# Kernel optimization log

Hardware: AMD Instinct MI355X
Metric: run time of the kernel (lower is better)

## Reference

```python
import jax, jax.numpy as jnp
import numpy as np

N, M, D = 131072, 128, 128

def setup_inputs() -> dict:
    key = jax.random.key(0)
    k1, k2, k3 = jax.random.split(key, 3)
    X = jax.random.normal(k1, (N, D), dtype=jnp.float32)
    r = jax.random.uniform(k2, (N, M), dtype=jnp.float32)
    mus = jax.random.normal(k3, (M, D), dtype=jnp.float32)
    return {"X": X, "r": r, "mus": mus}

def reference(X, r, mus):
    # Squared pairwise L2 distances without materializing [N, M, D]:
    x2 = jnp.sum(X * X, axis=1)            # [N]
    mu2 = jnp.sum(mus * mus, axis=1)       # [M]
    cross = X @ mus.T                      # [N, M]
    dist2 = jnp.maximum(x2[:, None] + mu2[None, :] - 2.0 * cross, 0.0)
    loss = jnp.sum(r * dist2) / X.shape[0]
    return loss
```

## Files before the change

### kernel.cpp

```cpp
#include <hip/hip_runtime.h>
#include <hip/hip_bf16.h>


typedef __attribute__((ext_vector_type(8)))  short  short8;
typedef __attribute__((ext_vector_type(16))) float  float16v;

#define LDSP 136

#if defined(__has_builtin)
#if __has_builtin(__builtin_amdgcn_cvt_pk_bf16_f32)
#define HAVE_PK_BF16 1
#endif
#endif

__device__ __forceinline__ unsigned int pk_bf16(float x, float y) {
#ifdef HAVE_PK_BF16
    typedef __attribute__((ext_vector_type(2))) __bf16 bf16x2;
    bf16x2 p = __builtin_amdgcn_cvt_pk_bf16_f32(x, y);
    return __builtin_bit_cast(unsigned int, p);
#else
    unsigned int ux = __float_as_uint(x);
    unsigned int uy = __float_as_uint(y);
    ux += 0x7fffu + ((ux >> 16) & 1u);
    uy += 0x7fffu + ((uy >> 16) & 1u);
    return (ux >> 16) | (uy & 0xffff0000u);
#endif
}

__global__ void zero_ws_kernel(float* ws) { ws[threadIdx.x] = 0.0f; }

__global__ void final_reduce_kernel(const float* ws, float* out) {
    const int lane = threadIdx.x;
    float t = ws[lane];
    #pragma unroll
    for (int off = 32; off > 0; off >>= 1) t += __shfl_down(t, off);
    if (lane == 0) out[0] = t * (1.0f / 131072.0f);
}

__global__ __launch_bounds__(256, 3)
void isoloss_kernel(const float* __restrict__ X,
                    const float* __restrict__ r,
                    const float* __restrict__ mus,
                    float* __restrict__ ws)
{
    const int tid  = threadIdx.x;
    const int blk  = blockIdx.x;
    const int wave = tid >> 6;
    const int lane = tid & 63;
    const int col  = lane & 31;
    const int half = lane >> 5;

    __shared__ unsigned short ldsA[128 * LDSP];
    __shared__ float x2s[128];
    __shared__ float wsum[4];

    const float* xbase = X + (size_t)blk * 128 * 128;
    float4 xv[16];
    #pragma unroll
    for (int it = 0; it < 16; ++it)
        xv[it] = *(const float4*)(xbase + (size_t)(it * 256 + tid) * 4);

    #pragma unroll
    for (int it = 0; it < 16; ++it) {
        const float4 v = xv[it];
        float p = v.x*v.x + v.y*v.y + v.z*v.z + v.w*v.w;
        p += __shfl_xor(p, 16);
        p += __shfl_xor(p, 8);
        p += __shfl_xor(p, 4);
        p += __shfl_xor(p, 2);
        p += __shfl_xor(p, 1);
        const int row = it * 8 + (tid >> 5);
        if ((tid & 31) == 0) x2s[row] = p;
        uint2 h;
        h.x = pk_bf16(v.x, v.y);
        h.y = pk_bf16(v.z, v.w);
        *(uint2*)&ldsA[row * LDSP + (tid & 31) * 4] = h;
    }

    short8 bfrag[8];
    float mu2p = 0.0f;
    {
        const float* mrow = mus + (size_t)(wave * 32 + col) * 128 + half * 8;
        #pragma unroll
        for (int ks = 0; ks < 8; ++ks) {
            const float4 a = *(const float4*)(mrow + ks * 16);
            const float4 b = *(const float4*)(mrow + ks * 16 + 4);
            mu2p += a.x*a.x + a.y*a.y + a.z*a.z + a.w*a.w
                  + b.x*b.x + b.y*b.y + b.z*b.z + b.w*b.w;
            union { short8 s8; uint4 u4; } u;
            u.u4.x = pk_bf16(a.x, a.y);
            u.u4.y = pk_bf16(a.z, a.w);
            u.u4.z = pk_bf16(b.x, b.y);
            u.u4.w = pk_bf16(b.z, b.w);
            bfrag[ks] = u.s8;
        }
    }
    const float mu2 = mu2p + __shfl_xor(mu2p, 32);

    __syncthreads();

    float s = 0.0f;
    #pragma unroll
    for (int mt = 0; mt < 4; ++mt) {
        const float* rp = r + (size_t)(blk * 128 + mt * 32) * 128 + wave * 32 + col;
        float rv[16];
        #pragma unroll
        for (int reg = 0; reg < 16; ++reg) {
            const int rl = (reg & 3) + 8 * (reg >> 2) + 4 * half;
            rv[reg] = rp[(size_t)rl * 128];
        }

        float16v acc = {};
        #pragma unroll
        for (int ks = 0; ks < 8; ++ks) {
            const short8 af = *(const short8*)&ldsA[(mt * 32 + col) * LDSP + ks * 16 + half * 8];
            acc = __builtin_amdgcn_mfma_f32_32x32x16_bf16(af, bfrag[ks], acc, 0, 0, 0);
        }

        float4 xq[4];
        #pragma unroll
        for (int q = 0; q < 4; ++q)
            xq[q] = *(const float4*)&x2s[mt * 32 + q * 8 + half * 4];

        #pragma unroll
        for (int reg = 0; reg < 16; ++reg) {
            const float d = fmaxf(xq[reg >> 2][reg & 3] + mu2 - 2.0f * acc[reg], 0.0f);
            s += rv[reg] * d;
        }
    }

    #pragma unroll
    for (int off = 32; off > 0; off >>= 1) s += __shfl_down(s, off);
    if (lane == 0) wsum[wave] = s;
    __syncthreads();
    if (tid == 0)
        atomicAdd(&ws[blk & 63], wsum[0] + wsum[1] + wsum[2] + wsum[3]);
}

extern "C" void kernel_launch(void* const* d_in, const int* in_sizes, int n_in,
                              void* d_out, int out_size, void* d_ws, size_t ws_size,
                              hipStream_t stream) {
    const float* X   = (const float*)d_in[0];
    const float* r   = (const float*)d_in[1];
    const float* mus = (const float*)d_in[2];
    float* out = (float*)d_out;
    float* ws  = (float*)d_ws;

    zero_ws_kernel<<<1, 64, 0, stream>>>(ws);
    isoloss_kernel<<<1024, 256, 0, stream>>>(X, r, mus, ws);
    final_reduce_kernel<<<1, 64, 0, stream>>>(ws, out);
}
```

Before: 151.0 us.

## Software-pipeline X/r loads across 32-row groups with double-buffered LDS

Replaces the up-front load of the whole 128x128 X tile with a loop over four 32-row groups. Each group uses a double-buffered LDS slice, and the next group's X and r are prefetched while the current group runs its MFMAs. The MFMA operands are swapped so that r can be read as contiguous float4 vectors, and a barrier that waits only on LDS (not on outstanding global loads) lets those loads stay in flight. LDS use drops and launch bounds rise to 4 blocks per CU for more occupancy, at the cost of more barriers per block and tighter register limits.

```diff
diff --git a/kernel.cpp b/kernel.cpp
--- a/kernel.cpp
+++ b/kernel.cpp
@@ -27,6 +27,13 @@
 #endif
 }
 
+__device__ __forceinline__ void barrier_lgkm_only() {
+    asm volatile("" ::: "memory");
+    __builtin_amdgcn_s_waitcnt(0xC07F);
+    __builtin_amdgcn_s_barrier();
+    asm volatile("" ::: "memory");
+}
+
 __global__ void zero_ws_kernel(float* ws) { ws[threadIdx.x] = 0.0f; }
 
 __global__ void final_reduce_kernel(const float* ws, float* out) {
@@ -37,7 +44,7 @@
     if (lane == 0) out[0] = t * (1.0f / 131072.0f);
 }
 
-__global__ __launch_bounds__(256, 3)
+__global__ __launch_bounds__(256, 4)
 void isoloss_kernel(const float* __restrict__ X,
                     const float* __restrict__ r,
                     const float* __restrict__ mus,
@@ -50,32 +57,9 @@
     const int col  = lane & 31;
     const int half = lane >> 5;
 
-    __shared__ unsigned short ldsA[128 * LDSP];
-    __shared__ float x2s[128];
+    __shared__ unsigned short ldsA[2][32 * LDSP];
+    __shared__ float x2s[2][32];
     __shared__ float wsum[4];
-
-    const float* xbase = X + (size_t)blk * 128 * 128;
-    float4 xv[16];
-    #pragma unroll
-    for (int it = 0; it < 16; ++it)
-        xv[it] = *(const float4*)(xbase + (size_t)(it * 256 + tid) * 4);
-
-    #pragma unroll
-    for (int it = 0; it < 16; ++it) {
-        const float4 v = xv[it];
-        float p = v.x*v.x + v.y*v.y + v.z*v.z + v.w*v.w;
-        p += __shfl_xor(p, 16);
-        p += __shfl_xor(p, 8);
-        p += __shfl_xor(p, 4);
-        p += __shfl_xor(p, 2);
-        p += __shfl_xor(p, 1);
-        const int row = it * 8 + (tid >> 5);
-        if ((tid & 31) == 0) x2s[row] = p;
-        uint2 h;
-        h.x = pk_bf16(v.x, v.y);
-        h.y = pk_bf16(v.z, v.w);
-        *(uint2*)&ldsA[row * LDSP + (tid & 31) * 4] = h;
-    }
 
     short8 bfrag[8];
     float mu2p = 0.0f;
@@ -96,36 +80,83 @@
         }
     }
     const float mu2 = mu2p + __shfl_xor(mu2p, 32);
+    float4 mu2q[4];
+    #pragma unroll
+    for (int q = 0; q < 4; ++q) {
+        mu2q[q].x = __shfl(mu2, q * 8 + half * 4 + 0);
+        mu2q[q].y = __shfl(mu2, q * 8 + half * 4 + 1);
+        mu2q[q].z = __shfl(mu2, q * 8 + half * 4 + 2);
+        mu2q[q].w = __shfl(mu2, q * 8 + half * 4 + 3);
+    }
 
-    __syncthreads();
+    const int g0 = blk * 4;
+    float4 xv[4], rv[4];
+    {
+        const float* xb = X + (size_t)g0 * 32 * 128;
+        #pragma unroll
+        for (int j = 0; j < 4; ++j)
+            xv[j] = *(const float4*)(xb + (size_t)(j * 256 + tid) * 4);
+        const float* rb = r + (size_t)(g0 * 32 + col) * 128 + wave * 32 + half * 4;
+        #pragma unroll
+        for (int q = 0; q < 4; ++q)
+            rv[q] = *(const float4*)(rb + q * 8);
+    }
 
     float s = 0.0f;
+
     #pragma unroll
-    for (int mt = 0; mt < 4; ++mt) {
-        const float* rp = r + (size_t)(blk * 128 + mt * 32) * 128 + wave * 32 + col;
-        float rv[16];
+    for (int g = 0; g < 4; ++g) {
+        const int buf = g & 1;
+
         #pragma unroll
-        for (int reg = 0; reg < 16; ++reg) {
-            const int rl = (reg & 3) + 8 * (reg >> 2) + 4 * half;
-            rv[reg] = rp[(size_t)rl * 128];
+        for (int j = 0; j < 4; ++j) {
+            const float4 v = xv[j];
+            float p = v.x*v.x + v.y*v.y + v.z*v.z + v.w*v.w;
+            p += __shfl_xor(p, 16);
+            p += __shfl_xor(p, 8);
+            p += __shfl_xor(p, 4);
+            p += __shfl_xor(p, 2);
+            p += __shfl_xor(p, 1);
+            const int row = j * 8 + (tid >> 5);
+            if ((tid & 31) == 0) x2s[buf][row] = p;
+            uint2 h;
+            h.x = pk_bf16(v.x, v.y);
+            h.y = pk_bf16(v.z, v.w);
+            *(uint2*)&ldsA[buf][row * LDSP + (tid & 31) * 4] = h;
         }
+
+        if (g < 3) {
+            const float* xb = X + (size_t)(g0 + g + 1) * 32 * 128;
+            #pragma unroll
+            for (int j = 0; j < 4; ++j)
+                xv[j] = *(const float4*)(xb + (size_t)(j * 256 + tid) * 4);
+        }
+
+        barrier_lgkm_only();
 
         float16v acc = {};
         #pragma unroll
         for (int ks = 0; ks < 8; ++ks) {
-            const short8 af = *(const short8*)&ldsA[(mt * 32 + col) * LDSP + ks * 16 + half * 8];
-            acc = __builtin_amdgcn_mfma_f32_32x32x16_bf16(af, bfrag[ks], acc, 0, 0, 0);
+            const short8 af = *(const short8*)&ldsA[buf][col * LDSP + ks * 16 + half * 8];
+            acc = __builtin_amdgcn_mfma_f32_32x32x16_bf16(bfrag[ks], af, acc, 0, 0, 0);
         }
 
-        float4 xq[4];
+        const float x2r = x2s[buf][col];
         #pragma unroll
-        for (int q = 0; q < 4; ++q)
-            xq[q] = *(const float4*)&x2s[mt * 32 + q * 8 + half * 4];
+        for (int q = 0; q < 4; ++q) {
+            const float4 rq = rv[q];
+            const float4 m2 = mu2q[q];
+            s += rq.x * fmaxf(x2r + m2.x - 2.0f * acc[q * 4 + 0], 0.0f);
+            s += rq.y * fmaxf(x2r + m2.y - 2.0f * acc[q * 4 + 1], 0.0f);
+            s += rq.z * fmaxf(x2r + m2.z - 2.0f * acc[q * 4 + 2], 0.0f);
+            s += rq.w * fmaxf(x2r + m2.w - 2.0f * acc[q * 4 + 3], 0.0f);
+        }
 
-        #pragma unroll
-        for (int reg = 0; reg < 16; ++reg) {
-            const float d = fmaxf(xq[reg >> 2][reg & 3] + mu2 - 2.0f * acc[reg], 0.0f);
-            s += rv[reg] * d;
+        if (g < 3) {
+            const float* rb = r + (size_t)((g0 + g + 1) * 32 + col) * 128 + wave * 32 + half * 4;
+            #pragma unroll
+            for (int q = 0; q < 4; ++q)
+                rv[q] = *(const float4*)(rb + q * 8);
         }
     }
 
```

After: 189.9 us. 25.8% more time.
